# Kernel optimization log

Measured on AMD Instinct MI355X. Metric: run time of the kernel, lower is better.

Reference implementation:

```python
import jax, jax.numpy as jnp
import numpy as np
from jax.scipy.linalg import expm

LATENT, HID, OMEGA, TRANZ, K = 64, 40, 9, 3, 262144


def _linear_params(key, out_d, in_d):
    # equinox Linear default init: U(-1/sqrt(in), 1/sqrt(in)) for weight and bias
    lim = 1.0 / np.sqrt(in_d)
    kw, kb = jax.random.split(key)
    W = jax.random.uniform(kw, (out_d, in_d), minval=-lim, maxval=lim, dtype=jnp.float32)
    b = jax.random.uniform(kb, (out_d,), minval=-lim, maxval=lim, dtype=jnp.float32)
    return W, b


def setup_inputs() -> dict:
    key = jax.random.key(0)
    keys = jax.random.split(key, 7)
    W_o1, b_o1 = _linear_params(keys[0], HID, LATENT)
    W_o2, b_o2 = _linear_params(keys[1], HID, HID)
    W_o3, b_o3 = _linear_params(keys[2], OMEGA, HID)
    W_t1, b_t1 = _linear_params(keys[3], HID, LATENT)
    W_t2, b_t2 = _linear_params(keys[4], HID, HID)
    W_t3, b_t3 = _linear_params(keys[5], TRANZ, HID)
    x = jax.random.normal(keys[6], (LATENT, K), dtype=jnp.float32)
    return {
        "x": x,
        "W_o1": W_o1, "b_o1": b_o1, "W_o2": W_o2, "b_o2": b_o2, "W_o3": W_o3, "b_o3": b_o3,
        "W_t1": W_t1, "b_t1": b_t1, "W_t2": W_t2, "b_t2": b_t2, "W_t3": W_t3, "b_t3": b_t3,
    }


def _exp_omega(omega_flat):
    # omega_flat: (9, K); expm of each column reshaped to 3x3, flattened -> (K, 9)
    f = lambda col: expm(col.reshape(3, 3)).reshape(9)
    return jax.vmap(f, in_axes=1)(omega_flat)


def reference(x, W_o1, b_o1, W_o2, b_o2, W_o3, b_o3,
              W_t1, b_t1, W_t2, b_t2, W_t3, b_t3):
    relu = jax.nn.relu
    # omega branch (note: original applies relu after EVERY layer, incl. last)
    h = relu(W_o1 @ x + b_o1[:, None])
    h = relu(W_o2 @ h + b_o2[:, None])
    omega = relu(W_o3 @ h + b_o3[:, None])          # (9, K)
    rotation = _exp_omega(omega).T                   # (9, K)
    # translation branch
    t = relu(W_t1 @ x + b_t1[:, None])
    t = relu(W_t2 @ t + b_t2[:, None])
    translation = relu(W_t3 @ t + b_t3[:, None])     # (3, K)
    return (omega, rotation, translation)
```

## Files before the change

### kernel.cpp

```cpp
#include <hip/hip_runtime.h>
#include <hip/hip_bf16.h>

#define KC 262144

typedef __attribute__((ext_vector_type(8))) short bf16x8;
typedef __attribute__((ext_vector_type(4))) float f32x4;
typedef unsigned short u16;
typedef unsigned int u32;

__device__ __forceinline__ u16 f2bf(float f) {
    u32 u = __float_as_uint(f);
    return (u16)((u + 0x7fffu + ((u >> 16) & 1u)) >> 16);
}
__device__ __forceinline__ u32 pk2(float a, float b) {
    u16 lo = __bfloat16_as_ushort(__float2bfloat16(a));
    u16 hi = __bfloat16_as_ushort(__float2bfloat16(b));
    return (u32)lo | ((u32)hi << 16);
}
__device__ __forceinline__ float bf2f(u32 h) {
    return __uint_as_float(h << 16);
}

__global__ __launch_bounds__(256) void prep(
    const float* __restrict__ Wo1, const float* __restrict__ bo1,
    const float* __restrict__ Wo2, const float* __restrict__ bo2,
    const float* __restrict__ Wo3, const float* __restrict__ bo3,
    const float* __restrict__ Wt1, const float* __restrict__ bt1,
    const float* __restrict__ Wt2, const float* __restrict__ bt2,
    const float* __restrict__ Wt3, const float* __restrict__ bt3,
    u16* __restrict__ ws)
{
    u16* W1s = ws;
    u16* W2s = ws + 5120;
    u16* W3s = ws + 12800;
    float* b1s = (float*)(ws + 14336);
    const int t0 = blockIdx.x * 256 + threadIdx.x;
    const int NT = gridDim.x * 256;

    for (int i = t0; i < 5120; i += NT) {
        int r = i >> 6, k = i & 63;
        float v = (r < 40) ? Wo1[r * 64 + k] : Wt1[(r - 40) * 64 + k];
        W1s[i] = f2bf(v);
    }
    for (int i = t0; i < 7680; i += NT) {
        int r = i / 96, k = i - r * 96;
        float v = 0.f;
        if (r < 40) {
            if (k < 40) v = Wo2[r * 40 + k];
            else if (k == 80) v = bo2[r];
        } else {
            int rr = r - 40;
            if (k >= 40 && k < 80) v = Wt2[rr * 40 + (k - 40)];
            else if (k == 80) v = bt2[rr];
        }
        W2s[i] = f2bf(v);
    }
    for (int i = t0; i < 1536; i += NT) {
        int r = i / 96, k = i - r * 96;
        float v = 0.f;
        if (r < 9) {
            if (k < 40) v = Wo3[r * 40 + k];
            else if (k == 80) v = bo3[r];
        } else if (r < 12) {
            int rr = r - 9;
            if (k >= 40 && k < 80) v = Wt3[rr * 40 + (k - 40)];
            else if (k == 80) v = bt3[rr];
        }
        W3s[i] = f2bf(v);
    }
    for (int i = t0; i < 80; i += NT)
        b1s[i] = (i < 40) ? bo1[i] : bt1[i - 40];
}

__global__ __launch_bounds__(256, 2) void mlp_mfma(
    const float* __restrict__ x, const u16* __restrict__ ws,
    float* __restrict__ out)
{
    const u16* W1s = ws;
    const u16* W2s = ws + 5120;
    const u16* W3s = ws + 12800;
    const float* b1s = (const float*)(ws + 14336);

    __shared__ u16 hst[4][16][120];
    __shared__ u16 l3s[4][64][18];

    const int tid = threadIdx.x;
    const int wid = tid >> 6;
    const int lane = tid & 63;
    const int g = lane >> 4;
    const int c = lane & 15;
    const int wgid = blockIdx.x * 4 + wid;
    const int cbase = wgid * 64;

    bf16x8 A1[5][2], A3[3];
    f32x4 b1v[5];
#pragma unroll
    for (int m = 0; m < 5; ++m) {
#pragma unroll
        for (int s = 0; s < 2; ++s)
            A1[m][s] = *(const bf16x8*)(W1s + (16 * m + c) * 64 + 32 * s + 8 * g);
        b1v[m] = *(const f32x4*)(b1s + 16 * m + 4 * g);
    }
    bf16x8 A2[5][3];
#pragma unroll
    for (int m = 0; m < 5; ++m)
#pragma unroll
        for (int s = 0; s < 3; ++s)
            if (!(s == 0 && m >= 3))
                A2[m][s] = *(const bf16x8*)(W2s + (16 * m + c) * 96 + 32 * s + 8 * g);
#pragma unroll
    for (int s = 0; s < 3; ++s)
        A3[s] = *(const bf16x8*)(W3s + c * 96 + 32 * s + 8 * g);

    {
        uint2 z;
        z.x = (g == 0) ? 0x00003f80u : 0u;
        z.y = 0u;
        *(uint2*)&hst[wid][c][80 + 4 * g] = z;
    }

    u32 xoff[16];
#pragma unroll
    for (int jj = 0; jj < 16; ++jj) {
        int row = 8 * g + (jj & 7) + 32 * (jj >> 3);
        xoff[jj] = (u32)((row * KC + cbase + c) * 4);
    }
    const char* xb_ = (const char*)x;

    float xr[16];
#pragma unroll
    for (int jj = 0; jj < 16; ++jj)
        xr[jj] = *(const float*)(xb_ + xoff[jj]);

#pragma unroll
    for (int t = 0; t < 4; ++t) {
        bf16x8 xv[2];
#pragma unroll
        for (int s = 0; s < 2; ++s) {
            union { u32 u[4]; bf16x8 v; } uu;
#pragma unroll
            for (int p = 0; p < 4; ++p)
                uu.u[p] = pk2(xr[8 * s + 2 * p], xr[8 * s + 2 * p + 1]);
            xv[s] = uu.v;
        }

        float xrn[16];
        if (t < 3) {
#pragma unroll
            for (int jj = 0; jj < 16; ++jj)
                xrn[jj] = *(const float*)(xb_ + (xoff[jj] + (t + 1) * 64));
        }

        f32x4 a1[5];
#pragma unroll
        for (int m = 0; m < 5; ++m) a1[m] = b1v[m];
#pragma unroll
        for (int s = 0; s < 2; ++s)
#pragma unroll
            for (int m = 0; m < 5; ++m)
                a1[m] = __builtin_amdgcn_mfma_f32_16x16x32_bf16(
                    A1[m][s], xv[s], a1[m], 0, 0, 0);
#pragma unroll
        for (int m = 0; m < 5; ++m) {
            uint2 w;
            w.x = pk2(fmaxf(a1[m][0], 0.f), fmaxf(a1[m][1], 0.f));
            w.y = pk2(fmaxf(a1[m][2], 0.f), fmaxf(a1[m][3], 0.f));
            *(uint2*)&hst[wid][c][16 * m + 4 * g] = w;
        }

        f32x4 a2[5];
#pragma unroll
        for (int m = 0; m < 5; ++m) a2[m] = f32x4{0.f, 0.f, 0.f, 0.f};
#pragma unroll
        for (int s = 0; s < 3; ++s) {
            bf16x8 hb = *(const bf16x8*)&hst[wid][c][32 * s + 8 * g];
#pragma unroll
            for (int m = 0; m < 5; ++m)
                if (!(s == 0 && m >= 3))
                    a2[m] = __builtin_amdgcn_mfma_f32_16x16x32_bf16(
                        A2[m][s], hb, a2[m], 0, 0, 0);
        }
#pragma unroll
        for (int m = 0; m < 5; ++m) {
            uint2 w;
            w.x = pk2(fmaxf(a2[m][0], 0.f), fmaxf(a2[m][1], 0.f));
            w.y = pk2(fmaxf(a2[m][2], 0.f), fmaxf(a2[m][3], 0.f));
            *(uint2*)&hst[wid][c][16 * m + 4 * g] = w;
        }

        f32x4 a3 = f32x4{0.f, 0.f, 0.f, 0.f};
#pragma unroll
        for (int s = 0; s < 3; ++s) {
            bf16x8 hb = *(const bf16x8*)&hst[wid][c][32 * s + 8 * g];
            a3 = __builtin_amdgcn_mfma_f32_16x16x32_bf16(
                A3[s], hb, a3, 0, 0, 0);
        }
        {
            uint2 w;
            w.x = pk2(fmaxf(a3[0], 0.f), fmaxf(a3[1], 0.f));
            w.y = pk2(fmaxf(a3[2], 0.f), fmaxf(a3[3], 0.f));
            *(uint2*)&l3s[wid][16 * t + c][4 * g] = w;
        }

        if (t < 3) {
#pragma unroll
            for (int jj = 0; jj < 16; ++jj)
                xr[jj] = xrn[jj];
        }
    }

    {
        uint4 q0 = *(const uint4*)&l3s[wid][lane][0];
        uint2 q1 = *(const uint2*)&l3s[wid][lane][8];
        float om[9];
        om[0] = bf2f(q0.x & 0xffffu); om[1] = bf2f(q0.x >> 16);
        om[2] = bf2f(q0.y & 0xffffu); om[3] = bf2f(q0.y >> 16);
        om[4] = bf2f(q0.z & 0xffffu); om[5] = bf2f(q0.z >> 16);
        om[6] = bf2f(q0.w & 0xffffu); om[7] = bf2f(q0.w >> 16);
        om[8] = bf2f(q1.x & 0xffffu);
        float tr0 = bf2f(q1.x >> 16);
        float tr1 = bf2f(q1.y & 0xffffu);
        float tr2 = bf2f(q1.y >> 16);

        const size_t ob = (size_t)cbase + lane;
#pragma unroll
        for (int j = 0; j < 9; ++j)
            out[(size_t)j * KC + ob] = om[j];
        out[(size_t)18 * KC + ob] = tr0;
        out[(size_t)19 * KC + ob] = tr1;
        out[(size_t)20 * KC + ob] = tr2;

        float B[9];
#pragma unroll
        for (int i = 0; i < 9; ++i) B[i] = om[i] * (1.0f / 32.0f);
        float T[9] = {1.f, 0.f, 0.f, 0.f, 1.f, 0.f, 0.f, 0.f, 1.f};
#pragma unroll
        for (int m = 9; m >= 1; --m) {
            float U[9];
#pragma unroll
            for (int rr = 0; rr < 3; ++rr)
#pragma unroll
                for (int cc = 0; cc < 3; ++cc)
                    U[rr * 3 + cc] = B[rr * 3 + 0] * T[0 * 3 + cc]
                                   + B[rr * 3 + 1] * T[1 * 3 + cc]
                                   + B[rr * 3 + 2] * T[2 * 3 + cc];
            const float s = 1.0f / (float)m;
#pragma unroll
            for (int i = 0; i < 9; ++i)
                T[i] = U[i] * s + ((i == 0 || i == 4 || i == 8) ? 1.0f : 0.0f);
        }
#pragma unroll
        for (int q = 0; q < 5; ++q) {
            float U[9];
#pragma unroll
            for (int rr = 0; rr < 3; ++rr)
#pragma unroll
                for (int cc = 0; cc < 3; ++cc)
                    U[rr * 3 + cc] = T[rr * 3 + 0] * T[0 * 3 + cc]
                                   + T[rr * 3 + 1] * T[1 * 3 + cc]
                                   + T[rr * 3 + 2] * T[2 * 3 + cc];
#pragma unroll
            for (int i = 0; i < 9; ++i) T[i] = U[i];
        }
#pragma unroll
        for (int j = 0; j < 9; ++j)
            out[(size_t)(9 + j) * KC + ob] = T[j];
    }
}

extern "C" void kernel_launch(void* const* d_in, const int* in_sizes, int n_in,
                              void* d_out, int out_size, void* d_ws, size_t ws_size,
                              hipStream_t stream) {
    const float* x   = (const float*)d_in[0];
    const float* Wo1 = (const float*)d_in[1];
    const float* bo1 = (const float*)d_in[2];
    const float* Wo2 = (const float*)d_in[3];
    const float* bo2 = (const float*)d_in[4];
    const float* Wo3 = (const float*)d_in[5];
    const float* bo3 = (const float*)d_in[6];
    const float* Wt1 = (const float*)d_in[7];
    const float* bt1 = (const float*)d_in[8];
    const float* Wt2 = (const float*)d_in[9];
    const float* bt2 = (const float*)d_in[10];
    const float* Wt3 = (const float*)d_in[11];
    const float* bt3 = (const float*)d_in[12];

    u16* ws = (u16*)d_ws;
    float* out = (float*)d_out;

    hipLaunchKernelGGL(prep, dim3(16), dim3(256), 0, stream,
                       Wo1, bo1, Wo2, bo2, Wo3, bo3,
                       Wt1, bt1, Wt2, bt2, Wt3, bt3, ws);
    hipLaunchKernelGGL(mlp_mfma, dim3(1024), dim3(256), 0, stream,
                       x, ws, out);
}
```

Measured before the change: 33.59 us.

## Fuse weight prep kernel into MLP kernel via per-block LDS staging

Removes the separate prep launch and has every block convert the fp32 weights to bf16 into shared memory itself, then load its MFMA fragments from LDS. The weight LDS region is reused for the hidden-activation and layer-3 staging buffers after a barrier. The x loads are issued before the weight conversion so their latency overlaps it. This drops one kernel launch and the dependency between kernels, but every one of 1024 blocks now repeats about 14K weight conversions and adds two block-wide barriers.

```diff
diff --git a/kernel.cpp b/kernel.cpp
--- a/kernel.cpp
+++ b/kernel.cpp
@@ -21,28 +21,51 @@
     return __uint_as_float(h << 16);
 }
 
-__global__ __launch_bounds__(256) void prep(
+__global__ __launch_bounds__(256, 2) void mlp_fused(
+    const float* __restrict__ x,
     const float* __restrict__ Wo1, const float* __restrict__ bo1,
     const float* __restrict__ Wo2, const float* __restrict__ bo2,
     const float* __restrict__ Wo3, const float* __restrict__ bo3,
     const float* __restrict__ Wt1, const float* __restrict__ bt1,
     const float* __restrict__ Wt2, const float* __restrict__ bt2,
     const float* __restrict__ Wt3, const float* __restrict__ bt3,
-    u16* __restrict__ ws)
+    float* __restrict__ out)
 {
-    u16* W1s = ws;
-    u16* W2s = ws + 5120;
-    u16* W3s = ws + 12800;
-    float* b1s = (float*)(ws + 14336);
-    const int t0 = blockIdx.x * 256 + threadIdx.x;
-    const int NT = gridDim.x * 256;
-
-    for (int i = t0; i < 5120; i += NT) {
+    __shared__ char lds[28992];
+    u16* W1s = (u16*)lds;
+    u16* W2s = W1s + 5120;
+    u16* W3s = W2s + 7680;
+    float* b1s = (float*)(W3s + 1536);
+
+    const int tid = threadIdx.x;
+    const int wid = tid >> 6;
+    const int lane = tid & 63;
+    const int g = lane >> 4;
+    const int c = lane & 15;
+    const int wgid = blockIdx.x * 4 + wid;
+    const int cbase = wgid * 64;
+
+    u16* hstp = (u16*)lds + wid * 1920;
+    u16* l3sp = (u16*)lds + 7680 + wid * 1152;
+
+    u32 xoff[16];
+#pragma unroll
+    for (int jj = 0; jj < 16; ++jj) {
+        int row = 8 * g + (jj & 7) + 32 * (jj >> 3);
+        xoff[jj] = (u32)((row * KC + cbase + c) * 4);
+    }
+    const char* xb_ = (const char*)x;
+    float xr[16];
+#pragma unroll
+    for (int jj = 0; jj < 16; ++jj)
+        xr[jj] = *(const float*)(xb_ + xoff[jj]);
+
+    for (int i = tid; i < 5120; i += 256) {
         int r = i >> 6, k = i & 63;
         float v = (r < 40) ? Wo1[r * 64 + k] : Wt1[(r - 40) * 64 + k];
         W1s[i] = f2bf(v);
     }
-    for (int i = t0; i < 7680; i += NT) {
+    for (int i = tid; i < 7680; i += 256) {
         int r = i / 96, k = i - r * 96;
         float v = 0.f;
         if (r < 40) {
@@ -55,7 +78,7 @@
         }
         W2s[i] = f2bf(v);
     }
-    for (int i = t0; i < 1536; i += NT) {
+    for (int i = tid; i < 1536; i += 256) {
         int r = i / 96, k = i - r * 96;
         float v = 0.f;
         if (r < 9) {
@@ -68,29 +91,10 @@
         }
         W3s[i] = f2bf(v);
     }
-    for (int i = t0; i < 80; i += NT)
+    for (int i = tid; i < 80; i += 256)
         b1s[i] = (i < 40) ? bo1[i] : bt1[i - 40];
-}
-
-__global__ __launch_bounds__(256, 2) void mlp_mfma(
-    const float* __restrict__ x, const u16* __restrict__ ws,
-    float* __restrict__ out)
-{
-    const u16* W1s = ws;
-    const u16* W2s = ws + 5120;
-    const u16* W3s = ws + 12800;
-    const float* b1s = (const float*)(ws + 14336);
-
-    __shared__ u16 hst[4][16][120];
-    __shared__ u16 l3s[4][64][18];
-
-    const int tid = threadIdx.x;
-    const int wid = tid >> 6;
-    const int lane = tid & 63;
-    const int g = lane >> 4;
-    const int c = lane & 15;
-    const int wgid = blockIdx.x * 4 + wid;
-    const int cbase = wgid * 64;
+
+    __syncthreads();
 
     bf16x8 A1[5][2], A3[3];
     f32x4 b1v[5];
@@ -111,26 +115,15 @@
 #pragma unroll
     for (int s = 0; s < 3; ++s)
         A3[s] = *(const bf16x8*)(W3s + c * 96 + 32 * s + 8 * g);
+
+    __syncthreads();
 
     {
         uint2 z;
         z.x = (g == 0) ? 0x00003f80u : 0u;
         z.y = 0u;
-        *(uint2*)&hst[wid][c][80 + 4 * g] = z;
-    }
-
-    u32 xoff[16];
-#pragma unroll
-    for (int jj = 0; jj < 16; ++jj) {
-        int row = 8 * g + (jj & 7) + 32 * (jj >> 3);
-        xoff[jj] = (u32)((row * KC + cbase + c) * 4);
-    }
-    const char* xb_ = (const char*)x;
-
-    float xr[16];
-#pragma unroll
-    for (int jj = 0; jj < 16; ++jj)
-        xr[jj] = *(const float*)(xb_ + xoff[jj]);
+        *(uint2*)&hstp[c * 120 + 80 + 4 * g] = z;
+    }
 
 #pragma unroll
     for (int t = 0; t < 4; ++t) {
@@ -165,7 +158,7 @@
             uint2 w;
             w.x = pk2(fmaxf(a1[m][0], 0.f), fmaxf(a1[m][1], 0.f));
             w.y = pk2(fmaxf(a1[m][2], 0.f), fmaxf(a1[m][3], 0.f));
-            *(uint2*)&hst[wid][c][16 * m + 4 * g] = w;
+            *(uint2*)&hstp[c * 120 + 16 * m + 4 * g] = w;
         }
 
         f32x4 a2[5];
@@ -173,7 +166,7 @@
         for (int m = 0; m < 5; ++m) a2[m] = f32x4{0.f, 0.f, 0.f, 0.f};
 #pragma unroll
         for (int s = 0; s < 3; ++s) {
-            bf16x8 hb = *(const bf16x8*)&hst[wid][c][32 * s + 8 * g];
+            bf16x8 hb = *(const bf16x8*)&hstp[c * 120 + 32 * s + 8 * g];
 #pragma unroll
             for (int m = 0; m < 5; ++m)
                 if (!(s == 0 && m >= 3))
@@ -185,13 +178,13 @@
             uint2 w;
             w.x = pk2(fmaxf(a2[m][0], 0.f), fmaxf(a2[m][1], 0.f));
             w.y = pk2(fmaxf(a2[m][2], 0.f), fmaxf(a2[m][3], 0.f));
-            *(uint2*)&hst[wid][c][16 * m + 4 * g] = w;
+            *(uint2*)&hstp[c * 120 + 16 * m + 4 * g] = w;
         }
 
         f32x4 a3 = f32x4{0.f, 0.f, 0.f, 0.f};
 #pragma unroll
         for (int s = 0; s < 3; ++s) {
-            bf16x8 hb = *(const bf16x8*)&hst[wid][c][32 * s + 8 * g];
+            bf16x8 hb = *(const bf16x8*)&hstp[c * 120 + 32 * s + 8 * g];
             a3 = __builtin_amdgcn_mfma_f32_16x16x32_bf16(
                 A3[s], hb, a3, 0, 0, 0);
         }
@@ -199,7 +192,7 @@
             uint2 w;
             w.x = pk2(fmaxf(a3[0], 0.f), fmaxf(a3[1], 0.f));
             w.y = pk2(fmaxf(a3[2], 0.f), fmaxf(a3[3], 0.f));
-            *(uint2*)&l3s[wid][16 * t + c][4 * g] = w;
+            *(uint2*)&l3sp[(16 * t + c) * 18 + 4 * g] = w;
         }
 
         if (t < 3) {
@@ -210,8 +203,8 @@
     }
 
     {
-        uint4 q0 = *(const uint4*)&l3s[wid][lane][0];
-        uint2 q1 = *(const uint2*)&l3s[wid][lane][8];
+        uint4 q0 = *(const uint4*)&l3sp[lane * 18];
+        uint2 q1 = *(const uint2*)&l3sp[lane * 18 + 8];
         float om[9];
         om[0] = bf2f(q0.x & 0xffffu); om[1] = bf2f(q0.x >> 16);
         om[2] = bf2f(q0.y & 0xffffu); om[3] = bf2f(q0.y >> 16);
@@ -233,7 +226,7 @@
         float B[9];
 #pragma unroll
         for (int i = 0; i < 9; ++i) B[i] = om[i] * (1.0f / 32.0f);
-        float T[9] = {1.f, 0.f, 0.f, 0.f, 1.f, 0.f, 0.f, 0.f, 1.f};
+        float T9[9] = {1.f, 0.f, 0.f, 0.f, 1.f, 0.f, 0.f, 0.f, 1.f};
 #pragma unroll
         for (int m = 9; m >= 1; --m) {
             float U[9];
@@ -241,13 +234,13 @@
             for (int rr = 0; rr < 3; ++rr)
 #pragma unroll
                 for (int cc = 0; cc < 3; ++cc)
-                    U[rr * 3 + cc] = B[rr * 3 + 0] * T[0 * 3 + cc]
-                                   + B[rr * 3 + 1] * T[1 * 3 + cc]
-                                   + B[rr * 3 + 2] * T[2 * 3 + cc];
+                    U[rr * 3 + cc] = B[rr * 3 + 0] * T9[0 * 3 + cc]
+                                   + B[rr * 3 + 1] * T9[1 * 3 + cc]
+                                   + B[rr * 3 + 2] * T9[2 * 3 + cc];
             const float s = 1.0f / (float)m;
 #pragma unroll
             for (int i = 0; i < 9; ++i)
-                T[i] = U[i] * s + ((i == 0 || i == 4 || i == 8) ? 1.0f : 0.0f);
+                T9[i] = U[i] * s + ((i == 0 || i == 4 || i == 8) ? 1.0f : 0.0f);
         }
 #pragma unroll
         for (int q = 0; q < 5; ++q) {
@@ -256,15 +249,15 @@
             for (int rr = 0; rr < 3; ++rr)
 #pragma unroll
                 for (int cc = 0; cc < 3; ++cc)
-                    U[rr * 3 + cc] = T[rr * 3 + 0] * T[0 * 3 + cc]
-                                   + T[rr * 3 + 1] * T[1 * 3 + cc]
-                                   + T[rr * 3 + 2] * T[2 * 3 + cc];
-#pragma unroll
-            for (int i = 0; i < 9; ++i) T[i] = U[i];
+                    U[rr * 3 + cc] = T9[rr * 3 + 0] * T9[0 * 3 + cc]
+                                   + T9[rr * 3 + 1] * T9[1 * 3 + cc]
+                                   + T9[rr * 3 + 2] * T9[2 * 3 + cc];
+#pragma unroll
+            for (int i = 0; i < 9; ++i) T9[i] = U[i];
         }
 #pragma unroll
         for (int j = 0; j < 9; ++j)
-            out[(size_t)(9 + j) * KC + ob] = T[j];
+            out[(size_t)(9 + j) * KC + ob] = T9[j];
     }
 }
 
@@ -285,12 +278,9 @@
     const float* Wt3 = (const float*)d_in[11];
     const float* bt3 = (const float*)d_in[12];
 
-    u16* ws = (u16*)d_ws;
     float* out = (float*)d_out;
 
-    hipLaunchKernelGGL(prep, dim3(16), dim3(256), 0, stream,
-                       Wo1, bo1, Wo2, bo2, Wo3, bo3,
-                       Wt1, bt1, Wt2, bt2, Wt3, bt3, ws);
-    hipLaunchKernelGGL(mlp_mfma, dim3(1024), dim3(256), 0, stream,
-                       x, ws, out);
-}
+    hipLaunchKernelGGL(mlp_fused, dim3(1024), dim3(256), 0, stream,
+                       x, Wo1, bo1, Wo2, bo2, Wo3, bo3,
+                       Wt1, bt1, Wt2, bt2, Wt3, bt3, out);
+}
```

After: 63.37 us. 1.89x slower.
